# Kernel tuning notes

Measured on AMD Instinct MI355X. Metric: run time of the kernel, lower is better.

The kernel has to match this reference:

```python
import jax, jax.numpy as jnp
import numpy as np

N, T, C, H, W = 16, 8, 256, 14, 14
IC = 64          # inter_channels
SCALE = 32       # nearest-upsample factor (scale_s); scale_t = 1


def setup_inputs() -> dict:
    key = jax.random.key(0)
    kx, kq1, kq2, kv1, kl, ki = jax.random.split(key, 6)
    cin = C + 1
    x = jax.random.normal(kx, (N, T, C, H, W), dtype=jnp.float32)
    lam = jax.random.uniform(kl, (), dtype=jnp.float32)
    index = jax.random.randint(ki, (N,), 0, N)
    # nn.Linear default init: U(-1/sqrt(fan_in), 1/sqrt(fan_in))
    bound = 1.0 / np.sqrt(cin)
    Wq = jax.random.uniform(kq1, (IC, cin), minval=-bound, maxval=bound, dtype=jnp.float32)
    bq = jax.random.uniform(kq2, (IC,), minval=-bound, maxval=bound, dtype=jnp.float32)
    Wv = jax.random.uniform(kv1, (1, cin), minval=-bound, maxval=bound, dtype=jnp.float32)
    Wv = Wv.at[0, C].set(4.0)   # value.weight.data[0, in_channel] = 4
    bv = jnp.zeros((1,), dtype=jnp.float32)  # value.bias.data[:] = 0
    return {"x": x, "lam": lam, "index": index, "Wq": Wq, "bq": bq, "Wv": Wv, "bv": bv}


def reference(x, lam, index, Wq, bq, Wv, bv):
    n, t, c, h, w = x.shape
    ic = Wq.shape[0]
    nt, hw = n * t, h * w
    x_lam = x.reshape(nt, c, h, w)
    x_lam_ = x[index].reshape(nt, c, h, w)           # batch-shuffled partner
    lam_block = jnp.broadcast_to(lam - 0.5, (nt, 1, h, w)).astype(x.dtype)
    x_lam = jnp.concatenate([x_lam, lam_block], axis=1)     # [nt, c+1, h, w]
    x_lam_ = jnp.concatenate([x_lam_, -lam_block], axis=1)
    # linear over channel dim (equivalent to the transpose(1,3)/Linear/transpose dance)
    q = jnp.einsum('nchw,dc->ndhw', x_lam, Wq) + bq[None, :, None, None]
    k = jnp.einsum('nchw,dc->ndhw', x_lam_, Wq) + bq[None, :, None, None]
    v = jnp.einsum('nchw,dc->ndhw', x_lam_, Wv) + bv[None, :, None, None]
    q_x = q.reshape(nt, ic, hw).transpose(0, 2, 1)   # [nt, hw, ic]
    k_x = k.reshape(nt, ic, hw)                      # [nt, ic, hw]
    v_ = v.reshape(nt, 1, hw).transpose(0, 2, 1)     # [nt, hw, 1]
    scores = jnp.einsum('nqd,ndk->nqk', q_x, k_x) / jnp.sqrt(jnp.float32(ic))
    attn = jax.nn.softmax(scores, axis=-1)           # [nt, hw, hw]
    mask_lam_ = jnp.matmul(attn.astype(jnp.float32), v_.astype(jnp.float32))
    mask_lam_ = mask_lam_.reshape(nt, 1, h, w)       # scale_t == 1 so expand is a no-op
    # F.interpolate(mode='nearest', scale_factor=SCALE)
    mask_lam_ = jnp.repeat(jnp.repeat(mask_lam_, SCALE, axis=2), SCALE, axis=3)
    mask_lam_ = jax.nn.sigmoid(mask_lam_)
    mask = jnp.concatenate([1.0 - mask_lam_, mask_lam_], axis=1)  # [nt, 2, h*S, w*S]
    v_out = v_.reshape(n, t, h, w)                    # (n, t*scale_t, h, w)
    return mask, v_out
```

## Files before the change

kernel.cpp:

```cpp
#include <hip/hip_runtime.h>
#include <hip/hip_bf16.h>
#include <stdint.h>

#define HWsz 196
#define MASK_ELEMS 51380224
#define VOUT_OFF   MASK_ELEMS

#define EQ_OFF_F 3221504
#define EK_OFF_F 4024704
#define V_OFF    4827904

typedef __attribute__((ext_vector_type(8))) short short8;
typedef __attribute__((ext_vector_type(4))) short short4v;
typedef __attribute__((ext_vector_type(4))) float f32x4;
typedef __attribute__((ext_vector_type(4))) uint32_t u32x4;

__device__ __forceinline__ bool is_bf16_mode(const void* wv) {
  return ((const uint16_t*)wv)[256] == (uint16_t)0x4080;
}

__device__ __forceinline__ float ldf(const void* p, int i, bool bf) {
  if (bf) {
    uint32_t u = (uint32_t)((const uint16_t*)p)[i] << 16;
    return __builtin_bit_cast(float, u);
  }
  return ((const float*)p)[i];
}

__device__ __forceinline__ uint16_t f2bf(float f) {
  __hip_bfloat16 h = __float2bfloat16(f);
  return __builtin_bit_cast(uint16_t, h);
}

__device__ __forceinline__ float bf2f(uint16_t u) {
  uint32_t v = (uint32_t)u << 16;
  return __builtin_bit_cast(float, v);
}

template<int NMT, int NCOLS, int J0>
__device__ __forceinline__ void k1_body(uint16_t* Abuf,
    const void* xraw, const int* index, const void* Wqraw, const void* bqraw,
    const void* Wvraw, const void* bvraw, const void* lamraw,
    float* ws, void* dout, int b) {
  int s = b & 127, isK = (b >> 7) & 1;
  int src = isK ? index[s >> 3] * 8 + (s & 7) : s;
  bool bf = is_bf16_mode(Wvraw);
  int tid = threadIdx.x;
  int lane = tid & 63, w = tid >> 6;
  int ln = lane & 15, quad = lane >> 4;
  int d = w * 16 + ln;
  size_t xbase = (size_t)src * 256 * 196;

  f32x4 acc[NMT];
#pragma unroll
  for (int mt = 0; mt < NMT; mt++) acc[mt] = (f32x4){0.f, 0.f, 0.f, 0.f};
  int cS1 = tid >> 2, jjS1 = tid & 3;
  uint32_t abase = (uint32_t)(uintptr_t)Abuf + (uint32_t)(quad * 128);

#pragma unroll 1
  for (int chunk = 0; chunk < 4; chunk++) {
    short8 bw0, bw1;
    {
      int cb = d * 257 + chunk * 64 + quad * 8;
#pragma unroll
      for (int e = 0; e < 8; e++) {
        bw0[e] = (short)f2bf(ldf(Wqraw, cb + e, bf));
        bw1[e] = (short)f2bf(ldf(Wqraw, cb + 32 + e, bf));
      }
    }
    __syncthreads();
    if (bf) {
      const uint16_t* xp = (const uint16_t*)xraw + xbase +
                           (size_t)(chunk * 64 + cS1) * 196 + J0;
      for (int jj = jjS1; jj * 4 < NCOLS; jj += 4)
        *(uint2*)(Abuf + (jj >> 2) * 1024 + cS1 * 16 + (jj & 3) * 4) =
            *(const uint2*)(xp + jj * 4);
    } else {
      const float* xp = (const float*)xraw + xbase +
                        (size_t)(chunk * 64 + cS1) * 196 + J0;
      for (int jj = jjS1; jj * 4 < NCOLS; jj += 4) {
        float4 v4 = *(const float4*)(xp + jj * 4);
        uint2 pk;
        pk.x = (uint32_t)f2bf(v4.x) | ((uint32_t)f2bf(v4.y) << 16);
        pk.y = (uint32_t)f2bf(v4.z) | ((uint32_t)f2bf(v4.w) << 16);
        *(uint2*)(Abuf + (jj >> 2) * 1024 + cS1 * 16 + (jj & 3) * 4) = pk;
      }
    }
    __syncthreads();
#pragma unroll
    for (int kc2 = 0; kc2 < 2; kc2++) {
      short4v lo[NMT], hi[NMT];
#pragma unroll
      for (int mt = 0; mt < NMT; mt++) {
        asm volatile("ds_read_b64_tr_b16 %0, %2 offset:%3\n\t"
                     "ds_read_b64_tr_b16 %1, %2 offset:%4"
                     : "=v"(lo[mt]), "=v"(hi[mt])
                     : "v"(abase), "i"(mt * 2048 + kc2 * 1024),
                       "i"(mt * 2048 + kc2 * 1024 + 128));
      }
      asm volatile("s_waitcnt lgkmcnt(0)" ::: "memory");
      __builtin_amdgcn_sched_barrier(0);
#pragma unroll
      for (int mt = 0; mt < NMT; mt++) {
        short8 af = __builtin_shufflevector(lo[mt], hi[mt], 0, 1, 2, 3, 4, 5, 6, 7);
        acc[mt] = __builtin_amdgcn_mfma_f32_16x16x32_bf16(af, kc2 ? bw1 : bw0,
                                                          acc[mt], 0, 0, 0);
      }
    }
  }

  float lamv = ldf(lamraw, 0, bf) - 0.5f;
  float lamch = isK ? -lamv : lamv;
  float addend = ldf(Wqraw, d * 257 + 256, bf) * lamch + ldf(bqraw, d, bf);
  __syncthreads();
#pragma unroll
  for (int mt = 0; mt < NMT; mt++) {
#pragma unroll
    for (int r = 0; r < 4; r++) {
      int jl = mt * 16 + quad * 4 + r;
      if (jl < NCOLS) Abuf[jl * 64 + d] = f2bf(acc[mt][r] + addend);
    }
  }
  __syncthreads();
  {
    uint16_t* E = (uint16_t*)(ws + (isK ? EK_OFF_F : EQ_OFF_F));
    const u32x4* As4 = (const u32x4*)Abuf;
    u32x4* Eg4 = (u32x4*)(E + (size_t)(s * HWsz + J0) * 64);
    for (int i = tid; i < NCOLS * 8; i += 256) Eg4[i] = As4[i];
  }

  if (isK && tid < NCOLS) {
    int j = J0 + tid;
    float vp0 = 0.f, vp1 = 0.f, vp2 = 0.f, vp3 = 0.f;
    if (bf) {
      const uint16_t* xp = (const uint16_t*)xraw + xbase + j;
#pragma unroll 4
      for (int c = 0; c < 256; c += 4) {
        vp0 = fmaf(bf2f(xp[(size_t)(c + 0) * 196]), ldf(Wvraw, c + 0, bf), vp0);
        vp1 = fmaf(bf2f(xp[(size_t)(c + 1) * 196]), ldf(Wvraw, c + 1, bf), vp1);
        vp2 = fmaf(bf2f(xp[(size_t)(c + 2) * 196]), ldf(Wvraw, c + 2, bf), vp2);
        vp3 = fmaf(bf2f(xp[(size_t)(c + 3) * 196]), ldf(Wvraw, c + 3, bf), vp3);
      }
    } else {
      const float* xp = (const float*)xraw + xbase + j;
#pragma unroll 4
      for (int c = 0; c < 256; c += 4) {
        vp0 = fmaf(xp[(size_t)(c + 0) * 196], ldf(Wvraw, c + 0, bf), vp0);
        vp1 = fmaf(xp[(size_t)(c + 1) * 196], ldf(Wvraw, c + 1, bf), vp1);
        vp2 = fmaf(xp[(size_t)(c + 2) * 196], ldf(Wvraw, c + 2, bf), vp2);
        vp3 = fmaf(xp[(size_t)(c + 3) * 196], ldf(Wvraw, c + 3, bf), vp3);
      }
    }
    float vvv = (vp0 + vp1) + (vp2 + vp3) + ldf(Wvraw, 256, bf) * lamch + ldf(bvraw, 0, bf);
    ws[V_OFF + s * HWsz + j] = vvv;
    if (bf) ((uint16_t*)dout)[VOUT_OFF + s * HWsz + j] = f2bf(vvv);
    else    ((float*)dout)[VOUT_OFF + s * HWsz + j] = vvv;
  }
}

__global__ __launch_bounds__(256) void k1_qk(const void* xraw, const int* index,
    const void* Wqraw, const void* bqraw, const void* Wvraw, const void* bvraw,
    const void* lamraw, float* ws, void* dout) {
  __shared__ __align__(16) uint16_t Abuf[7 * 1024];
  int b = blockIdx.x;
  if (b < 256)
    k1_body<7, 112, 0>(Abuf, xraw, index, Wqraw, bqraw, Wvraw, bvraw, lamraw, ws, dout, b);
  else
    k1_body<6, 84, 112>(Abuf, xraw, index, Wqraw, bqraw, Wvraw, bvraw, lamraw, ws, dout, b & 255);
}

__global__ __launch_bounds__(256) void k2_attn_mask(float* ws, void* dout, const void* Wvraw) {
  __shared__ float sig[64];
  bool bf = is_bf16_mode(Wvraw);
  int s = blockIdx.x >> 2, blk = blockIdx.x & 3;
  int tid = threadIdx.x;
  int lane = tid & 63, w = tid >> 6;
  int mt = blk * 4 + w;
  int ln = lane & 15, quad = lane >> 4;

  if (mt < 13) {
    const uint16_t* Eq = (const uint16_t*)(ws + EQ_OFF_F);
    const uint16_t* Ek = (const uint16_t*)(ws + EK_OFF_F);
    const uint16_t* qrow = Eq + ((size_t)s * 196 + mt * 16 + ln) * 64 + quad * 8;
    short8 aq0 = *(const short8*)(qrow);
    short8 aq1 = *(const short8*)(qrow + 32);

    float vcol[13];
    f32x4 acc[13];
#pragma unroll
    for (int nt = 0; nt < 13; nt++) {
      int col = nt * 16 + ln;
      vcol[nt] = (col < 196) ? ws[V_OFF + s * 196 + col] : 0.f;
      const uint16_t* krow = Ek + ((size_t)s * 196 + col) * 64 + quad * 8;
      short8 b0 = *(const short8*)(krow);
      short8 b1 = *(const short8*)(krow + 32);
      f32x4 a = (f32x4){0.f, 0.f, 0.f, 0.f};
      a = __builtin_amdgcn_mfma_f32_16x16x32_bf16(aq0, b0, a, 0, 0, 0);
      a = __builtin_amdgcn_mfma_f32_16x16x32_bf16(aq1, b1, a, 0, 0, 0);
      acc[nt] = a;
    }

    float mx[4] = {-1e30f, -1e30f, -1e30f, -1e30f};
#pragma unroll
    for (int nt = 0; nt < 13; nt++) {
      bool valid = (nt * 16 + ln) < 196;
#pragma unroll
      for (int r = 0; r < 4; r++) {
        float sv = valid ? acc[nt][r] * 0.125f : -1e30f;
        acc[nt][r] = sv;
        mx[r] = fmaxf(mx[r], sv);
      }
    }
#pragma unroll
    for (int m = 1; m < 16; m <<= 1)
#pragma unroll
      for (int r = 0; r < 4; r++) mx[r] = fmaxf(mx[r], __shfl_xor(mx[r], m));

    float l[4] = {0.f, 0.f, 0.f, 0.f}, av[4] = {0.f, 0.f, 0.f, 0.f};
#pragma unroll
    for (int nt = 0; nt < 13; nt++)
#pragma unroll
      for (int r = 0; r < 4; r++) {
        float p = __expf(acc[nt][r] - mx[r]);
        l[r] += p;
        av[r] += p * vcol[nt];
      }
#pragma unroll
    for (int m = 1; m < 16; m <<= 1)
#pragma unroll
      for (int r = 0; r < 4; r++) {
        l[r] += __shfl_xor(l[r], m);
        av[r] += __shfl_xor(av[r], m);
      }

    if (ln == 0) {
#pragma unroll
      for (int r = 0; r < 4; r++) {
        int j = mt * 16 + quad * 4 + r;
        if (j < 196) {
          float mval = av[r] / l[r];
          sig[j & 63] = 1.f / (1.f + __expf(-mval));
        }
      }
    }
  }
  __syncthreads();

  int j0 = blk * 64;
  int nrows = (blk == 3) ? 4 : 64;
  int base2 = s * 2;
  if (!bf) {
    float4* o4 = (float4*)dout;
    int total = nrows << 8;
    for (int i = tid; i < total; i += 256) {
      int x2 = i & 3, dy = (i >> 2) & 31, ch = (i >> 7) & 1, jl = i >> 8;
      int j = j0 + jl;
      int yhw = j / 14, xhw = j - yhw * 14;
      float v = sig[jl];
      if (!ch) v = 1.f - v;
      size_t off4 = (size_t)(base2 + ch) * 50176 +
                    (size_t)(yhw * 32 + dy) * 112 + (xhw << 3) + (x2 << 1);
      float4 f = make_float4(v, v, v, v);
      o4[off4] = f;
      o4[off4 + 1] = f;
    }
  } else {
    uint4* o = (uint4*)dout;
    int total = nrows << 7;
    for (int i = tid; i < total; i += 256) {
      int x2 = i & 1, dy = (i >> 1) & 31, ch = (i >> 6) & 1, jl = i >> 7;
      int j = j0 + jl;
      int yhw = j / 14, xhw = j - yhw * 14;
      float v = sig[jl];
      if (!ch) v = 1.f - v;
      uint32_t ub = (uint32_t)f2bf(v), pk = ub | (ub << 16);
      uint4 qv; qv.x = pk; qv.y = pk; qv.z = pk; qv.w = pk;
      size_t off = (size_t)(base2 + ch) * 25088 +
                   (size_t)(yhw * 32 + dy) * 56 + (xhw << 2) + (x2 << 1);
      o[off] = qv;
      o[off + 1] = qv;
    }
  }
}

extern "C" void kernel_launch(void* const* d_in, const int* in_sizes, int n_in,
                              void* d_out, int out_size, void* d_ws, size_t ws_size,
                              hipStream_t stream) {
  const void* x   = d_in[0];
  const void* lam = d_in[1];
  const int* idx  = (const int*)d_in[2];
  const void* Wq  = d_in[3];
  const void* bq  = d_in[4];
  const void* Wv  = d_in[5];
  const void* bv  = d_in[6];
  float* ws = (float*)d_ws;

  k1_qk<<<512, 256, 0, stream>>>(x, idx, Wq, bq, Wv, bv, lam, ws, d_out);
  k2_attn_mask<<<512, 256, 0, stream>>>(ws, d_out, Wv);
}
```

Baseline: 266.6 us.

## Derive K from shuffled Q projection instead of recomputing it

```diff
diff --git a/kernel.cpp b/kernel.cpp
--- a/kernel.cpp
+++ b/kernel.cpp
@@ -7,7 +7,6 @@
 #define VOUT_OFF   MASK_ELEMS
 
 #define EQ_OFF_F 3221504
-#define EK_OFF_F 4024704
 #define V_OFF    4827904
 
 typedef __attribute__((ext_vector_type(8))) short short8;
@@ -39,22 +38,21 @@
 
 template<int NMT, int NCOLS, int J0>
 __device__ __forceinline__ void k1_body(uint16_t* Abuf,
-    const void* xraw, const int* index, const void* Wqraw, const void* bqraw,
-    const void* Wvraw, const void* bvraw, const void* lamraw,
-    float* ws, void* dout, int b) {
-  int s = b & 127, isK = (b >> 7) & 1;
-  int src = isK ? index[s >> 3] * 8 + (s & 7) : s;
+    const void* xraw, const void* Wqraw, const void* bqraw,
+    const void* Wvraw, const void* lamraw, float* ws, int s) {
   bool bf = is_bf16_mode(Wvraw);
   int tid = threadIdx.x;
   int lane = tid & 63, w = tid >> 6;
   int ln = lane & 15, quad = lane >> 4;
   int d = w * 16 + ln;
-  size_t xbase = (size_t)src * 256 * 196;
+  size_t xbase = (size_t)s * 256 * 196;
 
   f32x4 acc[NMT];
 #pragma unroll
   for (int mt = 0; mt < NMT; mt++) acc[mt] = (f32x4){0.f, 0.f, 0.f, 0.f};
+  float vacc = 0.f;
   int cS1 = tid >> 2, jjS1 = tid & 3;
+  int vdB = (tid >> 4) * 1024 + (tid & 15);
   uint32_t abase = (uint32_t)(uintptr_t)Abuf + (uint32_t)(quad * 128);
 
 #pragma unroll 1
@@ -107,11 +105,15 @@
                                                           acc[mt], 0, 0, 0);
       }
     }
+    if (tid < NCOLS) {
+#pragma unroll 8
+      for (int c = 0; c < 64; c++)
+        vacc = fmaf(bf2f(Abuf[vdB + c * 16]), ldf(Wvraw, chunk * 64 + c, bf), vacc);
+    }
   }
 
   float lamv = ldf(lamraw, 0, bf) - 0.5f;
-  float lamch = isK ? -lamv : lamv;
-  float addend = ldf(Wqraw, d * 257 + 256, bf) * lamch + ldf(bqraw, d, bf);
+  float addend = ldf(Wqraw, d * 257 + 256, bf) * lamv + ldf(bqraw, d, bf);
   __syncthreads();
 #pragma unroll
   for (int mt = 0; mt < NMT; mt++) {
@@ -123,77 +125,69 @@
   }
   __syncthreads();
   {
-    uint16_t* E = (uint16_t*)(ws + (isK ? EK_OFF_F : EQ_OFF_F));
+    uint16_t* E = (uint16_t*)(ws + EQ_OFF_F);
     const u32x4* As4 = (const u32x4*)Abuf;
     u32x4* Eg4 = (u32x4*)(E + (size_t)(s * HWsz + J0) * 64);
     for (int i = tid; i < NCOLS * 8; i += 256) Eg4[i] = As4[i];
   }
 
-  if (isK && tid < NCOLS) {
-    int j = J0 + tid;
-    float vp0 = 0.f, vp1 = 0.f, vp2 = 0.f, vp3 = 0.f;
-    if (bf) {
-      const uint16_t* xp = (const uint16_t*)xraw + xbase + j;
-#pragma unroll 4
-      for (int c = 0; c < 256; c += 4) {
-        vp0 = fmaf(bf2f(xp[(size_t)(c + 0) * 196]), ldf(Wvraw, c + 0, bf), vp0);
-        vp1 = fmaf(bf2f(xp[(size_t)(c + 1) * 196]), ldf(Wvraw, c + 1, bf), vp1);
-        vp2 = fmaf(bf2f(xp[(size_t)(c + 2) * 196]), ldf(Wvraw, c + 2, bf), vp2);
-        vp3 = fmaf(bf2f(xp[(size_t)(c + 3) * 196]), ldf(Wvraw, c + 3, bf), vp3);
-      }
-    } else {
-      const float* xp = (const float*)xraw + xbase + j;
-#pragma unroll 4
-      for (int c = 0; c < 256; c += 4) {
-        vp0 = fmaf(xp[(size_t)(c + 0) * 196], ldf(Wvraw, c + 0, bf), vp0);
-        vp1 = fmaf(xp[(size_t)(c + 1) * 196], ldf(Wvraw, c + 1, bf), vp1);
-        vp2 = fmaf(xp[(size_t)(c + 2) * 196], ldf(Wvraw, c + 2, bf), vp2);
-        vp3 = fmaf(xp[(size_t)(c + 3) * 196], ldf(Wvraw, c + 3, bf), vp3);
-      }
-    }
-    float vvv = (vp0 + vp1) + (vp2 + vp3) + ldf(Wvraw, 256, bf) * lamch + ldf(bvraw, 0, bf);
-    ws[V_OFF + s * HWsz + j] = vvv;
-    if (bf) ((uint16_t*)dout)[VOUT_OFF + s * HWsz + j] = f2bf(vvv);
-    else    ((float*)dout)[VOUT_OFF + s * HWsz + j] = vvv;
-  }
-}
-
-__global__ __launch_bounds__(256) void k1_qk(const void* xraw, const int* index,
-    const void* Wqraw, const void* bqraw, const void* Wvraw, const void* bvraw,
-    const void* lamraw, float* ws, void* dout) {
+  if (tid < NCOLS) ws[V_OFF + s * HWsz + J0 + tid] = vacc;
+}
+
+__global__ __launch_bounds__(256) void k1_q(const void* xraw,
+    const void* Wqraw, const void* bqraw, const void* Wvraw,
+    const void* lamraw, float* ws) {
   __shared__ __align__(16) uint16_t Abuf[7 * 1024];
   int b = blockIdx.x;
-  if (b < 256)
-    k1_body<7, 112, 0>(Abuf, xraw, index, Wqraw, bqraw, Wvraw, bvraw, lamraw, ws, dout, b);
+  if (b < 128)
+    k1_body<7, 112, 0>(Abuf, xraw, Wqraw, bqraw, Wvraw, lamraw, ws, b);
   else
-    k1_body<6, 84, 112>(Abuf, xraw, index, Wqraw, bqraw, Wvraw, bvraw, lamraw, ws, dout, b & 255);
-}
-
-__global__ __launch_bounds__(256) void k2_attn_mask(float* ws, void* dout, const void* Wvraw) {
+    k1_body<6, 84, 112>(Abuf, xraw, Wqraw, bqraw, Wvraw, lamraw, ws, b & 127);
+}
+
+__global__ __launch_bounds__(256) void k2_attn_mask(float* ws, void* dout,
+    const void* Wvraw, const void* Wqraw, const void* lamraw,
+    const void* bvraw, const int* index) {
   __shared__ float sig[64];
   bool bf = is_bf16_mode(Wvraw);
   int s = blockIdx.x >> 2, blk = blockIdx.x & 3;
+  int src = index[s >> 3] * 8 + (s & 7);
   int tid = threadIdx.x;
   int lane = tid & 63, w = tid >> 6;
   int mt = blk * 4 + w;
   int ln = lane & 15, quad = lane >> 4;
+  float lamv = ldf(lamraw, 0, bf) - 0.5f;
+  float wv256 = ldf(Wvraw, 256, bf), bvv = ldf(bvraw, 0, bf);
 
   if (mt < 13) {
     const uint16_t* Eq = (const uint16_t*)(ws + EQ_OFF_F);
-    const uint16_t* Ek = (const uint16_t*)(ws + EK_OFF_F);
+    const uint16_t* Eqs = Eq + (size_t)src * 196 * 64;
     const uint16_t* qrow = Eq + ((size_t)s * 196 + mt * 16 + ln) * 64 + quad * 8;
     short8 aq0 = *(const short8*)(qrow);
     short8 aq1 = *(const short8*)(qrow + 32);
 
+    float dl0[8], dl1[8];
+#pragma unroll
+    for (int e = 0; e < 8; e++) {
+      dl0[e] = 2.f * lamv * ldf(Wqraw, (quad * 8 + e) * 257 + 256, bf);
+      dl1[e] = 2.f * lamv * ldf(Wqraw, (quad * 8 + e + 32) * 257 + 256, bf);
+    }
+
     float vcol[13];
     f32x4 acc[13];
 #pragma unroll
     for (int nt = 0; nt < 13; nt++) {
       int col = nt * 16 + ln;
-      vcol[nt] = (col < 196) ? ws[V_OFF + s * 196 + col] : 0.f;
-      const uint16_t* krow = Ek + ((size_t)s * 196 + col) * 64 + quad * 8;
-      short8 b0 = *(const short8*)(krow);
-      short8 b1 = *(const short8*)(krow + 32);
+      vcol[nt] = (col < 196) ? ws[V_OFF + src * 196 + col] - lamv * wv256 + bvv : 0.f;
+      const uint16_t* krow = Eqs + (size_t)col * 64 + quad * 8;
+      short8 b0r = *(const short8*)(krow);
+      short8 b1r = *(const short8*)(krow + 32);
+      short8 b0, b1;
+#pragma unroll
+      for (int e = 0; e < 8; e++) {
+        b0[e] = (short)f2bf(bf2f((uint16_t)b0r[e]) - dl0[e]);
+        b1[e] = (short)f2bf(bf2f((uint16_t)b1r[e]) - dl1[e]);
+      }
       f32x4 a = (f32x4){0.f, 0.f, 0.f, 0.f};
       a = __builtin_amdgcn_mfma_f32_16x16x32_bf16(aq0, b0, a, 0, 0, 0);
       a = __builtin_amdgcn_mfma_f32_16x16x32_bf16(aq1, b1, a, 0, 0, 0);
@@ -243,6 +237,12 @@
         }
       }
     }
+  }
+
+  if (blk == 0 && tid < 196) {
+    float vvv = ws[V_OFF + src * 196 + tid] - lamv * wv256 + bvv;
+    if (bf) ((uint16_t*)dout)[VOUT_OFF + s * HWsz + tid] = f2bf(vvv);
+    else    ((float*)dout)[VOUT_OFF + s * HWsz + tid] = vvv;
   }
   __syncthreads();
 
@@ -295,6 +295,6 @@
   const void* bv  = d_in[6];
   float* ws = (float*)d_ws;
 
-  k1_qk<<<512, 256, 0, stream>>>(x, idx, Wq, bq, Wv, bv, lam, ws, d_out);
-  k2_attn_mask<<<512, 256, 0, stream>>>(ws, d_out, Wv);
-}
+  k1_q<<<256, 256, 0, stream>>>(x, Wq, bq, Wv, lam, ws);
+  k2_attn_mask<<<512, 256, 0, stream>>>(ws, d_out, Wv, Wq, lam, bv, idx);
+}
```

Result: no change. 265.8 us (-0.3%).
